# Kernel tuning notes

Hardware: AMD Instinct MI355X
Metric: run time of the kernel (lower is better)

## Reference

```python
import jax, jax.numpy as jnp
import numpy as np

B, S, H, O = 128, 1000, 256, 2


def setup_inputs() -> dict:
    key = jax.random.key(0)
    ks = jax.random.split(key, 14)
    scale = 0.05
    return {
        "decoder_input": jax.random.normal(ks[0], (B, O), jnp.float32),
        "last_hidden": jax.random.normal(ks[1], (B, H), jnp.float32),
        "static": jax.random.normal(ks[2], (B, S, H), jnp.float32),
        "dynamic": jax.random.normal(ks[3], (B, S, H), jnp.float32),
        "emb_W": jax.random.normal(ks[4], (H, O), jnp.float32) * scale,
        "emb_b": jnp.zeros((H,), jnp.float32),
        "gru_Wih": jax.random.normal(ks[5], (3 * H, H), jnp.float32) * scale,
        "gru_Whh": jax.random.normal(ks[6], (3 * H, H), jnp.float32) * scale,
        "gru_bih": jnp.zeros((3 * H,), jnp.float32),
        "gru_bhh": jnp.zeros((3 * H,), jnp.float32),
        "attn_W": jax.random.normal(ks[7], (3 * H, 3 * H), jnp.float32) * scale,
        "attn_v": jax.random.normal(ks[8], (3 * H,), jnp.float32) * scale,
        "dec_W": jax.random.normal(ks[9], (2 * H, 2 * H), jnp.float32) * scale,
        "dec_v": jax.random.normal(ks[10], (2 * H,), jnp.float32) * scale,
    }


def _gru_cell(x, h, Wih, Whh, bih, bhh):
    # PyTorch GRU gate order: r, z, n
    gx = x @ Wih.T + bih          # [B, 3H]
    gh = h @ Whh.T + bhh          # [B, 3H]
    xr, xz, xn = jnp.split(gx, 3, axis=-1)
    hr, hz, hn = jnp.split(gh, 3, axis=-1)
    r = jax.nn.sigmoid(xr + hr)
    z = jax.nn.sigmoid(xz + hz)
    n = jnp.tanh(xn + r * hn)
    return (1.0 - z) * n + z * h


def reference(decoder_input, last_hidden, static, dynamic,
              emb_W, emb_b, gru_Wih, gru_Whh, gru_bih, gru_bhh,
              attn_W, attn_v, dec_W, dec_v):
    # Embed decoder input and run one GRU step
    embedded = decoder_input @ emb_W.T + emb_b                      # [B, H]
    h_new = _gru_cell(embedded, last_hidden, gru_Wih, gru_Whh, gru_bih, gru_bhh)  # [B, H]

    # Attention: v . tanh(W @ concat(static, dynamic, hidden)) per (b, s)
    hid = jnp.broadcast_to(h_new[:, None, :], static.shape)         # [B, S, H]
    cat = jnp.concatenate([static, dynamic, hid], axis=-1)          # [B, S, 3H]
    scores = jnp.tanh(jnp.einsum('bsk,jk->bsj', cat, attn_W)) @ attn_v  # [B, S]
    attn = jax.nn.softmax(scores, axis=1)

    # Context: attention-weighted sum of static encodings
    context = jnp.einsum('bs,bsh->bh', attn, static)                # [B, H]

    # Final pointer scorer over concat(static, context)
    ctx = jnp.broadcast_to(context[:, None, :], static.shape)
    cat2 = jnp.concatenate([static, ctx], axis=-1)                  # [B, S, 2H]
    out_scores = jnp.tanh(jnp.einsum('bsk,jk->bsj', cat2, dec_W)) @ dec_v  # [B, S]
    outputs = jax.nn.softmax(out_scores, axis=1)
    hidden = h_new[None]                                            # [1, B, H]
    return outputs, hidden
```

## Files before the change

### kernel.cpp

```cpp
#include <hip/hip_runtime.h>

#define BB 128
#define SS 1000
#define HH 256
#define H3 768
#define H2 512

typedef unsigned short u16;
typedef short short8 __attribute__((ext_vector_type(8)));
typedef float floatx4 __attribute__((ext_vector_type(4)));
typedef u16 ushort4v __attribute__((ext_vector_type(4)));

__device__ __forceinline__ u16 f2bf(float f) {
    unsigned int x = __float_as_uint(f);
    x += 0x7FFFu + ((x >> 16) & 1u);
    return (u16)(x >> 16);
}

__device__ __forceinline__ float fast_tanh(float x) {
    float t = __expf(2.0f * x);
    return 1.0f - 2.0f * __builtin_amdgcn_rcpf(t + 1.0f);
}

__device__ __forceinline__ float sigmoidf(float x) {
    return __builtin_amdgcn_rcpf(1.0f + __expf(-x));
}

__device__ __forceinline__ void gl2lds16(const void* src, void* dst) {
    __builtin_amdgcn_global_load_lds(
        (const __attribute__((address_space(1))) unsigned int*)src,
        (__attribute__((address_space(3))) unsigned int*)dst,
        16, 0, 0);
}

__global__ __launch_bounds__(256) void k_prep(
    const float* __restrict__ aW, const float* __restrict__ dW,
    u16* __restrict__ aWb, u16* __restrict__ dWb)
{
    int idx = (blockIdx.x * 256 + threadIdx.x) * 4;
    const float* src;
    u16* dst;
    if (idx < 589824) { src = aW + idx; dst = aWb + idx; }
    else              { src = dW + (idx - 589824); dst = dWb + (idx - 589824); }
    float4 v = *(const float4*)src;
    ushort4v o = { f2bf(v.x), f2bf(v.y), f2bf(v.z), f2bf(v.w) };
    *(ushort4v*)dst = o;
}

__global__ __launch_bounds__(256) void k_gru(
    const float* __restrict__ dec, const float* __restrict__ h0,
    const float* __restrict__ embW, const float* __restrict__ embb,
    const float* __restrict__ Wih, const float* __restrict__ Whh,
    const float* __restrict__ bih, const float* __restrict__ bhh,
    const float* __restrict__ attnW,
    float* __restrict__ Wh, float* __restrict__ out_hidden)
{
    const int b = blockIdx.x, t = threadIdx.x;
    __shared__ float emb_s[HH], h_s[HH], hn_s[HH];

    const float d0 = dec[b * 2 + 0], d1 = dec[b * 2 + 1];
    emb_s[t] = d0 * embW[t * 2 + 0] + d1 * embW[t * 2 + 1] + embb[t];
    h_s[t] = h0[b * HH + t];
    __syncthreads();

    auto dotrow = [&](const float* Wr, const float* xs) -> float {
        float acc = 0.f;
        const float4* p = (const float4*)Wr;
#pragma unroll 8
        for (int c = 0; c < HH / 4; ++c) {
            float4 w = p[c];
            acc += w.x * xs[c * 4 + 0] + w.y * xs[c * 4 + 1]
                 + w.z * xs[c * 4 + 2] + w.w * xs[c * 4 + 3];
        }
        return acc;
    };

    float gr = dotrow(Wih + (size_t)t * HH, emb_s) + bih[t]
             + dotrow(Whh + (size_t)t * HH, h_s) + bhh[t];
    float r = sigmoidf(gr);

    float gz = dotrow(Wih + (size_t)(HH + t) * HH, emb_s) + bih[HH + t]
             + dotrow(Whh + (size_t)(HH + t) * HH, h_s) + bhh[HH + t];
    float z = sigmoidf(gz);

    float xn = dotrow(Wih + (size_t)(2 * HH + t) * HH, emb_s) + bih[2 * HH + t];
    float hn = dotrow(Whh + (size_t)(2 * HH + t) * HH, h_s) + bhh[2 * HH + t];
    float n = fast_tanh(xn + r * hn);

    float hv = (1.0f - z) * n + z * h_s[t];
    out_hidden[b * HH + t] = hv;
    hn_s[t] = hv;
    __syncthreads();

#pragma unroll
    for (int rr = 0; rr < 3; ++rr) {
        int j = t + rr * HH;
        Wh[b * H3 + j] = dotrow(attnW + (size_t)j * H3 + 2 * HH, hn_s);
    }
}

template <int KSTEPS, int NTILES, int WSTRIDE>
__global__ __launch_bounds__(256, 2) void k_scores(
    const float* __restrict__ A1, const float* __restrict__ A2,
    const u16* __restrict__ Wb, const float* __restrict__ addj,
    const float* __restrict__ vj, float* __restrict__ out)
{
    constexpr int GPR    = KSTEPS * 4;
    constexpr int NINSTR = KSTEPS / 2;
    constexpr int BUFU16 = 1024 * KSTEPS;
    constexpr int NG     = NTILES / 2;

    __shared__ u16 smem[2 * BUFU16];

    const int b = blockIdx.y, t = threadIdx.x;
    const int wave = t >> 6, lane = t & 63;
    const int q = lane >> 4, c = lane & 15;
    const int swz = c & 7;
    const int s_base = blockIdx.x * 128 + wave * 32;
    const int kb = q * 8;

    short8 afrag[2][KSTEPS];
#pragma unroll
    for (int mt = 0; mt < 2; ++mt) {
        int row = s_base + mt * 16 + c;
        if (row > SS - 1) row = SS - 1;
        const size_t abase = (size_t)(b * SS + row) * HH;
#pragma unroll
        for (int ks = 0; ks < KSTEPS; ++ks) {
            int k = ks * 32 + kb;
            const float* src = (k < HH) ? (A1 + abase + k) : (A2 + abase + (k - HH));
            float4 u0 = *(const float4*)src;
            float4 u1 = *(const float4*)(src + 4);
            short8 f;
            f[0] = (short)f2bf(u0.x); f[1] = (short)f2bf(u0.y);
            f[2] = (short)f2bf(u0.z); f[3] = (short)f2bf(u0.w);
            f[4] = (short)f2bf(u1.x); f[5] = (short)f2bf(u1.y);
            f[6] = (short)f2bf(u1.z); f[7] = (short)f2bf(u1.w);
            afrag[mt][ks] = f;
        }
    }

    auto stage = [&](int g, int bufsel) {
        const int jbase = g * 32;
        u16* base = smem + bufsel * BUFU16;
#pragma unroll
        for (int i = 0; i < NINSTR; ++i) {
            int gl = (wave * NINSTR + i) * 64 + lane;
            int r  = gl / GPR;
            int p  = gl % GPR;
            int gg = p ^ (r & 7);
            const u16* src = Wb + (size_t)(jbase + r) * WSTRIDE + gg * 8;
            u16* dst = base + (size_t)(wave * NINSTR + i) * 512;
            gl2lds16(src, dst);
        }
    };

    float pout[2][4] = {{0.f, 0.f, 0.f, 0.f}, {0.f, 0.f, 0.f, 0.f}};

    stage(0, 0);
    for (int g = 0; g < NG; ++g) {
        __syncthreads();
        if (g + 1 < NG) stage(g + 1, (g + 1) & 1);

        const u16* base = smem + (g & 1) * BUFU16;
        floatx4 acc[2][2] = {{{0.f,0.f,0.f,0.f},{0.f,0.f,0.f,0.f}},
                             {{0.f,0.f,0.f,0.f},{0.f,0.f,0.f,0.f}}};
#pragma unroll
        for (int ks = 0; ks < KSTEPS; ++ks) {
            const int pg = ks * 4 + q;
#pragma unroll
            for (int jt = 0; jt < 2; ++jt) {
                const int paddr = ((jt * 16 + c) * GPR + (pg ^ swz)) * 8;
                short8 wf = *(const short8*)(base + paddr);
                acc[jt][0] = __builtin_amdgcn_mfma_f32_16x16x32_bf16(afrag[0][ks], wf, acc[jt][0], 0, 0, 0);
                acc[jt][1] = __builtin_amdgcn_mfma_f32_16x16x32_bf16(afrag[1][ks], wf, acc[jt][1], 0, 0, 0);
            }
        }
#pragma unroll
        for (int jt = 0; jt < 2; ++jt) {
            const int j = g * 32 + jt * 16 + c;
            const float aj = addj[b * (NTILES * 16) + j];
            const float vv = vj[j];
#pragma unroll
            for (int r4 = 0; r4 < 4; ++r4) {
                pout[0][r4] += fast_tanh(acc[jt][0][r4] + aj) * vv;
                pout[1][r4] += fast_tanh(acc[jt][1][r4] + aj) * vv;
            }
        }
    }

#pragma unroll
    for (int mt = 0; mt < 2; ++mt)
#pragma unroll
        for (int r4 = 0; r4 < 4; ++r4)
#pragma unroll
            for (int off = 1; off < 16; off <<= 1)
                pout[mt][r4] += __shfl_xor(pout[mt][r4], off, 64);

    if (c == 0) {
#pragma unroll
        for (int mt = 0; mt < 2; ++mt) {
            const int srow = s_base + mt * 16 + q * 4;
#pragma unroll
            for (int r4 = 0; r4 < 4; ++r4)
                if (srow + r4 < SS) out[b * SS + srow + r4] = pout[mt][r4];
        }
    }
}

__global__ __launch_bounds__(256) void k_softmax(
    const float* __restrict__ in, float* __restrict__ outf)
{
    const int b = blockIdx.x, t = threadIdx.x;
    __shared__ float red[4];
    const float* rowp = in + b * SS;

    float m = -1e30f;
    for (int s = t; s < SS; s += 256) m = fmaxf(m, rowp[s]);
#pragma unroll
    for (int off = 32; off >= 1; off >>= 1) m = fmaxf(m, __shfl_xor(m, off, 64));
    if ((t & 63) == 0) red[t >> 6] = m;
    __syncthreads();
    m = fmaxf(fmaxf(red[0], red[1]), fmaxf(red[2], red[3]));

    float sum = 0.f;
    for (int s = t; s < SS; s += 256) sum += __expf(rowp[s] - m);
#pragma unroll
    for (int off = 32; off >= 1; off >>= 1) sum += __shfl_xor(sum, off, 64);
    __syncthreads();
    if ((t & 63) == 0) red[t >> 6] = sum;
    __syncthreads();
    sum = red[0] + red[1] + red[2] + red[3];

    const float inv = 1.0f / sum;
    for (int s = t; s < SS; s += 256)
        outf[b * SS + s] = __expf(rowp[s] - m) * inv;
}

__global__ __launch_bounds__(256) void k_context(
    const float* __restrict__ attn, const float* __restrict__ stat,
    const float* __restrict__ decW, float* __restrict__ Dc)
{
    const int b = blockIdx.x, t = threadIdx.x;
    __shared__ float attn_s[SS];
    __shared__ float ctx_s[HH];
    for (int s = t; s < SS; s += 256) attn_s[s] = attn[b * SS + s];
    __syncthreads();

    float acc = 0.f;
    const float* base = stat + (size_t)b * SS * HH + t;
#pragma unroll 4
    for (int s = 0; s < SS; ++s) acc += attn_s[s] * base[(size_t)s * HH];
    ctx_s[t] = acc;
    __syncthreads();

#pragma unroll
    for (int rr = 0; rr < 2; ++rr) {
        int j = t + rr * 256;
        float a2 = 0.f;
        const float4* p = (const float4*)(decW + (size_t)j * H2 + HH);
#pragma unroll 8
        for (int cc = 0; cc < HH / 4; ++cc) {
            float4 w = p[cc];
            a2 += w.x * ctx_s[cc * 4 + 0] + w.y * ctx_s[cc * 4 + 1]
                + w.z * ctx_s[cc * 4 + 2] + w.w * ctx_s[cc * 4 + 3];
        }
        Dc[b * H2 + j] = a2;
    }
}

extern "C" void kernel_launch(void* const* d_in, const int* in_sizes, int n_in,
                              void* d_out, int out_size, void* d_ws, size_t ws_size,
                              hipStream_t stream)
{
    const float* dec   = (const float*)d_in[0];
    const float* h0    = (const float*)d_in[1];
    const float* stat  = (const float*)d_in[2];
    const float* dyn   = (const float*)d_in[3];
    const float* embW  = (const float*)d_in[4];
    const float* embb  = (const float*)d_in[5];
    const float* Wih   = (const float*)d_in[6];
    const float* Whh   = (const float*)d_in[7];
    const float* bih   = (const float*)d_in[8];
    const float* bhh   = (const float*)d_in[9];
    const float* attnW = (const float*)d_in[10];
    const float* attnv = (const float*)d_in[11];
    const float* decW  = (const float*)d_in[12];
    const float* decv  = (const float*)d_in[13];

    float* out        = (float*)d_out;
    float* out_probs  = out;
    float* out_hidden = out + BB * SS;

    u16* wsb     = (u16*)d_ws;
    u16* attnWb  = wsb;
    u16* decWb   = wsb + 589824;
    float* wsf   = (float*)(wsb + 851968);
    float* Wh      = wsf;
    float* scores  = wsf + 98304;
    float* attn    = wsf + 226304;
    float* Dc      = wsf + 354304;
    float* oscores = wsf + 419840;

    k_prep<<<832, 256, 0, stream>>>(attnW, decW, attnWb, decWb);
    k_gru<<<BB, 256, 0, stream>>>(dec, h0, embW, embb, Wih, Whh, bih, bhh,
                                  attnW, Wh, out_hidden);
    k_scores<16, 48, H3><<<dim3(8, BB), 256, 0, stream>>>(stat, dyn, attnWb, Wh,
                                                          attnv, scores);
    k_softmax<<<BB, 256, 0, stream>>>(scores, attn);
    k_context<<<BB, 256, 0, stream>>>(attn, stat, decW, Dc);
    k_scores<8, 32, H2><<<dim3(8, BB), 256, 0, stream>>>(stat, nullptr, decWb, Dc,
                                                         decv, oscores);
    k_softmax<<<BB, 256, 0, stream>>>(oscores, out_probs);
}
```

Baseline: 673.9 us.

## Pipeline MFMA epilogue with LDS prefetch and split context reduction across chunks

The scores kernel now issues the first weight-tile stage before the activation loads. It caches the per-row add and v vectors in shared memory and software-pipelines the LDS fragment reads. The tanh epilogue of the previous tile runs while the next tile's MFMAs are issued, using double-buffered accumulators. The context kernel, which used only 128 blocks, is split into a chunked partial-sum kernel over the sequence plus a reduction kernel that reads bf16 decoder weights. The goal is more parallelism on the bandwidth-bound context pass, at the cost of an extra launch, more registers, and bf16 rounding in the Dc projection.

```diff
diff --git a/kernel.cpp b/kernel.cpp
--- a/kernel.cpp
+++ b/kernel.cpp
@@ -5,11 +5,18 @@
 #define HH 256
 #define H3 768
 #define H2 512
+#define NCHUNK 8
 
 typedef unsigned short u16;
 typedef short short8 __attribute__((ext_vector_type(8)));
 typedef float floatx4 __attribute__((ext_vector_type(4)));
 typedef u16 ushort4v __attribute__((ext_vector_type(4)));
+
+__device__ __forceinline__ float bf2f(u16 u) {
+    union { unsigned int i; float f; } v;
+    v.i = ((unsigned int)u) << 16;
+    return v.f;
+}
 
 __device__ __forceinline__ u16 f2bf(float f) {
     unsigned int x = __float_as_uint(f);
@@ -109,8 +116,10 @@
     constexpr int NINSTR = KSTEPS / 2;
     constexpr int BUFU16 = 1024 * KSTEPS;
     constexpr int NG     = NTILES / 2;
+    constexpr int NJ     = NTILES * 16;
 
     __shared__ u16 smem[2 * BUFU16];
+    __shared__ float aj_s[NJ], vj_s[NJ];
 
     const int b = blockIdx.y, t = threadIdx.x;
     const int wave = t >> 6, lane = t & 63;
@@ -118,6 +127,27 @@
     const int swz = c & 7;
     const int s_base = blockIdx.x * 128 + wave * 32;
     const int kb = q * 8;
+
+    auto stage = [&](int g, int bufsel) {
+        const int jbase = g * 32;
+        u16* base = smem + bufsel * BUFU16;
+#pragma unroll
+        for (int i = 0; i < NINSTR; ++i) {
+            int gl = (wave * NINSTR + i) * 64 + lane;
+            int r  = gl / GPR;
+            int p  = gl % GPR;
+            int gg = p ^ (r & 7);
+            const u16* src = Wb + (size_t)(jbase + r) * WSTRIDE + gg * 8;
+            u16* dst = base + (size_t)(wave * NINSTR + i) * 512;
+            gl2lds16(src, dst);
+        }
+    };
+    stage(0, 0);
+
+    for (int i = t; i < NJ; i += 256) {
+        aj_s[i] = addj[b * NJ + i];
+        vj_s[i] = vj[i];
+    }
 
     short8 afrag[2][KSTEPS];
 #pragma unroll
@@ -140,54 +170,60 @@
         }
     }
 
-    auto stage = [&](int g, int bufsel) {
-        const int jbase = g * 32;
-        u16* base = smem + bufsel * BUFU16;
-#pragma unroll
-        for (int i = 0; i < NINSTR; ++i) {
-            int gl = (wave * NINSTR + i) * 64 + lane;
-            int r  = gl / GPR;
-            int p  = gl % GPR;
-            int gg = p ^ (r & 7);
-            const u16* src = Wb + (size_t)(jbase + r) * WSTRIDE + gg * 8;
-            u16* dst = base + (size_t)(wave * NINSTR + i) * 512;
-            gl2lds16(src, dst);
+    float pout[2][4] = {{0.f, 0.f, 0.f, 0.f}, {0.f, 0.f, 0.f, 0.f}};
+    floatx4 accB[2][2][2];
+
+    auto epilogue = [&](int gg) {
+        floatx4 (*ac)[2] = accB[gg & 1];
+#pragma unroll
+        for (int jt = 0; jt < 2; ++jt) {
+            const int j = gg * 32 + jt * 16 + c;
+            const float aj = aj_s[j];
+            const float vv = vj_s[j];
+#pragma unroll
+            for (int r4 = 0; r4 < 4; ++r4) {
+                pout[0][r4] += fast_tanh(ac[jt][0][r4] + aj) * vv;
+                pout[1][r4] += fast_tanh(ac[jt][1][r4] + aj) * vv;
+            }
         }
     };
 
-    float pout[2][4] = {{0.f, 0.f, 0.f, 0.f}, {0.f, 0.f, 0.f, 0.f}};
-
-    stage(0, 0);
+    int have = 0, gP = 0;
     for (int g = 0; g < NG; ++g) {
         __syncthreads();
         if (g + 1 < NG) stage(g + 1, (g + 1) & 1);
 
         const u16* base = smem + (g & 1) * BUFU16;
-        floatx4 acc[2][2] = {{{0.f,0.f,0.f,0.f},{0.f,0.f,0.f,0.f}},
-                             {{0.f,0.f,0.f,0.f},{0.f,0.f,0.f,0.f}}};
+        floatx4 (*acc)[2] = accB[g & 1];
+#pragma unroll
+        for (int jt = 0; jt < 2; ++jt)
+#pragma unroll
+            for (int mt = 0; mt < 2; ++mt)
+                acc[jt][mt] = (floatx4){0.f, 0.f, 0.f, 0.f};
+
+        auto ldsrd = [&](int ks, int jt) -> short8 {
+            const int paddr = ((jt * 16 + c) * GPR + ((ks * 4 + q) ^ swz)) * 8;
+            return *(const short8*)(base + paddr);
+        };
+
+        short8 wf0 = ldsrd(0, 0);
+        short8 wf1 = ldsrd(0, 1);
+
+        if (have) epilogue(gP);
+
 #pragma unroll
         for (int ks = 0; ks < KSTEPS; ++ks) {
-            const int pg = ks * 4 + q;
-#pragma unroll
-            for (int jt = 0; jt < 2; ++jt) {
-                const int paddr = ((jt * 16 + c) * GPR + (pg ^ swz)) * 8;
-                short8 wf = *(const short8*)(base + paddr);
-                acc[jt][0] = __builtin_amdgcn_mfma_f32_16x16x32_bf16(afrag[0][ks], wf, acc[jt][0], 0, 0, 0);
-                acc[jt][1] = __builtin_amdgcn_mfma_f32_16x16x32_bf16(afrag[1][ks], wf, acc[jt][1], 0, 0, 0);
-            }
-        }
-#pragma unroll
-        for (int jt = 0; jt < 2; ++jt) {
-            const int j = g * 32 + jt * 16 + c;
-            const float aj = addj[b * (NTILES * 16) + j];
-            const float vv = vj[j];
-#pragma unroll
-            for (int r4 = 0; r4 < 4; ++r4) {
-                pout[0][r4] += fast_tanh(acc[jt][0][r4] + aj) * vv;
-                pout[1][r4] += fast_tanh(acc[jt][1][r4] + aj) * vv;
-            }
-        }
-    }
+            short8 nf0, nf1;
+            if (ks + 1 < KSTEPS) { nf0 = ldsrd(ks + 1, 0); nf1 = ldsrd(ks + 1, 1); }
+            acc[0][0] = __builtin_amdgcn_mfma_f32_16x16x32_bf16(afrag[0][ks], wf0, acc[0][0], 0, 0, 0);
+            acc[0][1] = __builtin_amdgcn_mfma_f32_16x16x32_bf16(afrag[1][ks], wf0, acc[0][1], 0, 0, 0);
+            acc[1][0] = __builtin_amdgcn_mfma_f32_16x16x32_bf16(afrag[0][ks], wf1, acc[1][0], 0, 0, 0);
+            acc[1][1] = __builtin_amdgcn_mfma_f32_16x16x32_bf16(afrag[1][ks], wf1, acc[1][1], 0, 0, 0);
+            wf0 = nf0; wf1 = nf1;
+        }
+        gP = g; have = 1;
+    }
+    epilogue(gP);
 
 #pragma unroll
     for (int mt = 0; mt < 2; ++mt)
@@ -237,33 +273,58 @@
         outf[b * SS + s] = __expf(rowp[s] - m) * inv;
 }
 
-__global__ __launch_bounds__(256) void k_context(
+__global__ __launch_bounds__(256) void k_ctx_part(
     const float* __restrict__ attn, const float* __restrict__ stat,
-    const float* __restrict__ decW, float* __restrict__ Dc)
+    float* __restrict__ part)
+{
+    constexpr int CH = SS / NCHUNK;
+    const int chunk = blockIdx.x, b = blockIdx.y, t = threadIdx.x;
+    const int wave = t >> 6, lane = t & 63;
+
+    __shared__ float attn_s[CH];
+    __shared__ float red[4][HH];
+
+    for (int i = t; i < CH; i += 256) attn_s[i] = attn[b * SS + chunk * CH + i];
+    __syncthreads();
+
+    float4 acc = {0.f, 0.f, 0.f, 0.f};
+    const float* base = stat + ((size_t)(b * SS + chunk * CH) * HH) + lane * 4;
+#pragma unroll 4
+    for (int i = wave; i < CH; i += 4) {
+        float w = attn_s[i];
+        float4 v = *(const float4*)(base + (size_t)i * HH);
+        acc.x += w * v.x; acc.y += w * v.y; acc.z += w * v.z; acc.w += w * v.w;
+    }
+    *(float4*)(&red[wave][lane * 4]) = acc;
+    __syncthreads();
+
+    part[(size_t)(chunk * BB + b) * HH + t] =
+        red[0][t] + red[1][t] + red[2][t] + red[3][t];
+}
+
+__global__ __launch_bounds__(256) void k_ctx_red(
+    const float* __restrict__ part, const u16* __restrict__ decWb,
+    float* __restrict__ Dc)
 {
     const int b = blockIdx.x, t = threadIdx.x;
-    __shared__ float attn_s[SS];
     __shared__ float ctx_s[HH];
-    for (int s = t; s < SS; s += 256) attn_s[s] = attn[b * SS + s];
-    __syncthreads();
-
-    float acc = 0.f;
-    const float* base = stat + (size_t)b * SS * HH + t;
-#pragma unroll 4
-    for (int s = 0; s < SS; ++s) acc += attn_s[s] * base[(size_t)s * HH];
-    ctx_s[t] = acc;
+
+    float s = 0.f;
+#pragma unroll
+    for (int c = 0; c < NCHUNK; ++c) s += part[(size_t)(c * BB + b) * HH + t];
+    ctx_s[t] = s;
     __syncthreads();
 
 #pragma unroll
     for (int rr = 0; rr < 2; ++rr) {
         int j = t + rr * 256;
         float a2 = 0.f;
-        const float4* p = (const float4*)(decW + (size_t)j * H2 + HH);
-#pragma unroll 8
-        for (int cc = 0; cc < HH / 4; ++cc) {
-            float4 w = p[cc];
-            a2 += w.x * ctx_s[cc * 4 + 0] + w.y * ctx_s[cc * 4 + 1]
-                + w.z * ctx_s[cc * 4 + 2] + w.w * ctx_s[cc * 4 + 3];
+        const short8* p = (const short8*)(decWb + (size_t)j * H2 + HH);
+#pragma unroll 4
+        for (int cc = 0; cc < HH / 8; ++cc) {
+            short8 w = p[cc];
+#pragma unroll
+            for (int k = 0; k < 8; ++k) a2 += bf2f((u16)w[k]) * ctx_s[cc * 8 + k];
         }
         Dc[b * H2 + j] = a2;
     }
@@ -301,6 +362,7 @@
     float* attn    = wsf + 226304;
     float* Dc      = wsf + 354304;
     float* oscores = wsf + 419840;
+    float* ctxpart = wsf + 547840;
 
     k_prep<<<832, 256, 0, stream>>>(attnW, decW, attnWb, decWb);
     k_gru<<<BB, 256, 0, stream>>>(dec, h0, embW, embb, Wih, Whh, bih, bhh,
@@ -308,7 +370,8 @@
     k_scores<16, 48, H3><<<dim3(8, BB), 256, 0, stream>>>(stat, dyn, attnWb, Wh,
                                                           attnv, scores);
     k_softmax<<<BB, 256, 0, stream>>>(scores, attn);
-    k_context<<<BB, 256, 0, stream>>>(attn, stat, decW, Dc);
+    k_ctx_part<<<dim3(NCHUNK, BB), 256, 0, stream>>>(attn, stat, ctxpart);
+    k_ctx_red<<<BB, 256, 0, stream>>>(ctxpart, decWb, Dc);
     k_scores<8, 32, H2><<<dim3(8, BB), 256, 0, stream>>>(stat, nullptr, decWb, Dc,
                                                          decv, oscores);
     k_softmax<<<BB, 256, 0, stream>>>(oscores, out_probs);
```

Result: faster. 608.9 us (-9.7%).
